# Kernel optimization log

Hardware: AMD Instinct MI355X
Metric: run time of the kernel (lower is better)

Reference implementation:

```python
import jax, jax.numpy as jnp
import numpy as np

N, D = 8192, 1024

def setup_inputs() -> dict:
    key = jax.random.key(0)
    ks = jax.random.split(key, 7)
    s = 1.0 / np.sqrt(D)  # mimic nn.Linear init scale
    return {
        "embeddings": jax.random.normal(ks[0], (N, D), jnp.float32),
        "Wq": jax.random.normal(ks[1], (D, D), jnp.float32) * s,
        "bq": jax.random.normal(ks[2], (D,), jnp.float32) * s,
        "Wk": jax.random.normal(ks[3], (D, D), jnp.float32) * s,
        "bk": jax.random.normal(ks[4], (D,), jnp.float32) * s,
        "Wv": jax.random.normal(ks[5], (D, D), jnp.float32) * s,
        "bv": jax.random.normal(ks[6], (D,), jnp.float32) * s,
    }

def reference(embeddings, Wq, bq, Wk, bk, Wv, bv):
    # nn.Linear: y = x @ W^T + b; weights here are stored as [out, in] equivalent (square), use x @ W.T
    q = embeddings @ Wq.T + bq          # [N, D]
    k = embeddings @ Wk.T + bk          # [N, D]
    v = embeddings @ Wv.T + bv          # [N, D]
    scores = q @ k.T                    # [N, N]  (unscaled, as in source)
    attn = jax.nn.softmax(scores, axis=-1)
    out = attn @ v                      # [N, D]
    return out[:, None, :]              # [N, 1, D] matching torch broadcasted-matmul output
```

## Files before the change

kernel.cpp:

```cpp
#include <hip/hip_runtime.h>
#include <hip/hip_fp16.h>
#include <cstdint>
#include <cstddef>

typedef _Float16 half8 __attribute__((ext_vector_type(8)));
typedef _Float16 half4 __attribute__((ext_vector_type(4)));
typedef float floatx16 __attribute__((ext_vector_type(16)));

#define N_TOK 8192
#define DIM   1024

#define EPI_F32   0
#define EPI_PART  1

__device__ __forceinline__ void async_tile16(const _Float16* gp, _Float16* lp) {
    __builtin_amdgcn_global_load_lds(
        (const __attribute__((address_space(1))) void*)gp,
        (__attribute__((address_space(3))) void*)lp, 16, 0, 0);
}

template<int BM, int BN, int BK, bool ASPLIT, int EPI, bool REMAP>
__global__ __launch_bounds__(256)
void gemm_f16(const _Float16* __restrict__ Ahi, const _Float16* __restrict__ Alo,
              const _Float16* __restrict__ B,
              int kslice, int lda, int ldb,
              float* __restrict__ C, int ldc)
{
    constexpr int MI = BM / 64;
    constexpr int NI = BN / 64;
    constexpr int CPR = BK / 8;
    constexpr int SW  = CPR - 1;
    constexpr int RPP = 2048 / BK;
    constexpr int IA  = BM * BK / 2048;
    constexpr int IB  = BN * BK / 2048;
    constexpr int A_ELTS = BM * BK;
    constexpr int B_ELTS = BN * BK;
    __shared__ _Float16 smem[(ASPLIT ? 2 : 1) * A_ELTS + B_ELTS];
    constexpr int tAhi = 0;
    constexpr int tAlo = A_ELTS;
    constexpr int tB   = (ASPLIT ? 2 : 1) * A_ELTS;

    int bx = blockIdx.x, by = blockIdx.y, bz = blockIdx.z;
    if constexpr (REMAP) {
        const int gx = gridDim.x, gy = gridDim.y;
        const int gxy = gx * gy;
        const int nb = gxy * gridDim.z;
        const int bid = bz * gxy + by * gx + bx;
        const int nid = (bid & 7) * (nb >> 3) + (bid >> 3);
        bx = nid % gx; by = (nid / gx) % gy; bz = nid / gxy;
    }

    const int tid  = threadIdx.x;
    const int row0 = by * BM;
    const int col0 = bx * BN;
    const int lane = tid & 63;
    const int w    = tid >> 6;
    const int wm   = w & 1, wn = w >> 1;
    const int l31  = lane & 31, lhi = lane >> 5;

    floatx16 acc[MI][NI];
#pragma unroll
    for (int mi = 0; mi < MI; mi++)
#pragma unroll
        for (int ni = 0; ni < NI; ni++)
#pragma unroll
            for (int e = 0; e < 16; e++) acc[mi][ni][e] = 0.f;

    const int r_s = tid / CPR;
    const int j_s = tid % CPR;

    const int k_beg = bz * kslice;
    for (int k0 = k_beg; k0 < k_beg + kslice; k0 += BK) {
        __syncthreads();
#pragma unroll
        for (int i = 0; i < IA; i++) {
            const int r = i * RPP + r_s;
            const int jg = j_s ^ ((r >> 1) & SW);
            async_tile16(Ahi + (size_t)(row0 + r) * lda + k0 + jg * 8,
                         smem + tAhi + (i * 256 + tid) * 8);
            if constexpr (ASPLIT)
                async_tile16(Alo + (size_t)(row0 + r) * lda + k0 + jg * 8,
                             smem + tAlo + (i * 256 + tid) * 8);
        }
#pragma unroll
        for (int i = 0; i < IB; i++) {
            const int r = i * RPP + r_s;
            const int jg = j_s ^ ((r >> 1) & SW);
            async_tile16(B + (size_t)(col0 + r) * ldb + k0 + jg * 8,
                         smem + tB + (i * 256 + tid) * 8);
        }
        __syncthreads();

#pragma unroll
        for (int ks = 0; ks < BK / 16; ks++) {
            half8 af[MI], bf[NI];
            half8 al[ASPLIT ? MI : 1];
            const int cb = ks * 2 + lhi;
#pragma unroll
            for (int mi = 0; mi < MI; mi++) {
                const int r = wm * (BM / 2) + mi * 32 + l31;
                const int cj = (cb ^ ((r >> 1) & SW)) * 8;
                af[mi] = *(half8*)&smem[tAhi + r * BK + cj];
                if constexpr (ASPLIT) al[mi] = *(half8*)&smem[tAlo + r * BK + cj];
            }
#pragma unroll
            for (int ni = 0; ni < NI; ni++) {
                const int r = wn * (BN / 2) + ni * 32 + l31;
                const int cj = (cb ^ ((r >> 1) & SW)) * 8;
                bf[ni] = *(half8*)&smem[tB + r * BK + cj];
            }
#pragma unroll
            for (int mi = 0; mi < MI; mi++)
#pragma unroll
                for (int ni = 0; ni < NI; ni++) {
                    acc[mi][ni] = __builtin_amdgcn_mfma_f32_32x32x16_f16(af[mi], bf[ni], acc[mi][ni], 0, 0, 0);
                    if constexpr (ASPLIT)
                        acc[mi][ni] = __builtin_amdgcn_mfma_f32_32x32x16_f16(al[mi], bf[ni], acc[mi][ni], 0, 0, 0);
                }
        }
    }

#pragma unroll
    for (int mi = 0; mi < MI; mi++) {
#pragma unroll
        for (int ni = 0; ni < NI; ni++) {
            const int colg = col0 + wn * (BN / 2) + ni * 32 + l31;
            const int base = row0 + wm * (BM / 2) + mi * 32 + 4 * lhi;
#pragma unroll
            for (int g = 0; g < 4; g++) {
                const int rowb = base + 8 * g;
#pragma unroll
                for (int r2 = 0; r2 < 4; r2++) {
                    const int rowg = rowb + r2;
                    const float v = acc[mi][ni][4 * g + r2];
                    if constexpr (EPI == EPI_F32) {
                        C[(size_t)rowg * ldc + colg] = v;
                    } else {
                        C[(size_t)rowg * ldc + (size_t)bz * DIM + colg] = v;
                    }
                }
            }
        }
    }
}

template<int BM, int BN, int BK>
__global__ __launch_bounds__(256)
void gemm_qkv(const _Float16* __restrict__ Ehi, const _Float16* __restrict__ Elo,
              const _Float16* __restrict__ W,
              _Float16* __restrict__ qhi, _Float16* __restrict__ qlo,
              _Float16* __restrict__ khi, _Float16* __restrict__ vtr,
              const float* __restrict__ bq, const float* __restrict__ bk,
              const float* __restrict__ bv)
{
    constexpr int MI = BM / 64;
    constexpr int NI = BN / 64;
    constexpr int CPR = BK / 8;
    constexpr int SW  = CPR - 1;
    constexpr int RPP = 2048 / BK;
    constexpr int IA  = BM * BK / 2048;
    constexpr int IB  = BN * BK / 2048;
    constexpr int A_ELTS = BM * BK;
    constexpr int B_ELTS = BN * BK;
    __shared__ _Float16 smem[2 * A_ELTS + B_ELTS];
    constexpr int tAhi = 0;
    constexpr int tAlo = A_ELTS;
    constexpr int tB   = 2 * A_ELTS;

    int bx = blockIdx.x, by = blockIdx.y, bz = blockIdx.z;
    {
        const int gx = gridDim.x, gy = gridDim.y;
        const int gxy = gx * gy;
        const int nb = gxy * gridDim.z;
        const int bid = bz * gxy + by * gx + bx;
        const int nid = (bid & 7) * (nb >> 3) + (bid >> 3);
        bx = nid % gx; by = (nid / gx) % gy; bz = nid / gxy;
    }
    const int unit = bz;
    const bool dolo = (unit < 2);

    const int tid  = threadIdx.x;
    const int row0 = by * BM;
    const int col0 = bx * BN;
    const int lane = tid & 63;
    const int w    = tid >> 6;
    const int wm   = w & 1, wn = w >> 1;
    const int l31  = lane & 31, lhi = lane >> 5;

    floatx16 acc[MI][NI];
#pragma unroll
    for (int mi = 0; mi < MI; mi++)
#pragma unroll
        for (int ni = 0; ni < NI; ni++)
#pragma unroll
            for (int e = 0; e < 16; e++) acc[mi][ni][e] = 0.f;

    const int r_s = tid / CPR;
    const int j_s = tid % CPR;
    const size_t brow0 = (size_t)(unit * DIM + col0);

    for (int k0 = 0; k0 < DIM; k0 += BK) {
        __syncthreads();
#pragma unroll
        for (int i = 0; i < IA; i++) {
            const int r = i * RPP + r_s;
            const int jg = j_s ^ ((r >> 1) & SW);
            async_tile16(Ehi + (size_t)(row0 + r) * DIM + k0 + jg * 8,
                         smem + tAhi + (i * 256 + tid) * 8);
            if (dolo)
                async_tile16(Elo + (size_t)(row0 + r) * DIM + k0 + jg * 8,
                             smem + tAlo + (i * 256 + tid) * 8);
        }
#pragma unroll
        for (int i = 0; i < IB; i++) {
            const int r = i * RPP + r_s;
            const int jg = j_s ^ ((r >> 1) & SW);
            async_tile16(W + (brow0 + r) * DIM + k0 + jg * 8,
                         smem + tB + (i * 256 + tid) * 8);
        }
        __syncthreads();

#pragma unroll
        for (int ks = 0; ks < BK / 16; ks++) {
            half8 af[MI], bf[NI], al[MI];
            const int cb = ks * 2 + lhi;
#pragma unroll
            for (int mi = 0; mi < MI; mi++) {
                const int r = wm * (BM / 2) + mi * 32 + l31;
                const int cj = (cb ^ ((r >> 1) & SW)) * 8;
                af[mi] = *(half8*)&smem[tAhi + r * BK + cj];
                if (dolo) al[mi] = *(half8*)&smem[tAlo + r * BK + cj];
            }
#pragma unroll
            for (int ni = 0; ni < NI; ni++) {
                const int r = wn * (BN / 2) + ni * 32 + l31;
                const int cj = (cb ^ ((r >> 1) & SW)) * 8;
                bf[ni] = *(half8*)&smem[tB + r * BK + cj];
            }
#pragma unroll
            for (int mi = 0; mi < MI; mi++)
#pragma unroll
                for (int ni = 0; ni < NI; ni++)
                    acc[mi][ni] = __builtin_amdgcn_mfma_f32_32x32x16_f16(af[mi], bf[ni], acc[mi][ni], 0, 0, 0);
            if (dolo) {
#pragma unroll
                for (int mi = 0; mi < MI; mi++)
#pragma unroll
                    for (int ni = 0; ni < NI; ni++)
                        acc[mi][ni] = __builtin_amdgcn_mfma_f32_32x32x16_f16(al[mi], bf[ni], acc[mi][ni], 0, 0, 0);
            }
        }
    }

    const float* bias = (unit == 0) ? bq : (unit == 1) ? bk : bv;
#pragma unroll
    for (int mi = 0; mi < MI; mi++) {
#pragma unroll
        for (int ni = 0; ni < NI; ni++) {
            const int colg = col0 + wn * (BN / 2) + ni * 32 + l31;
            const float bb = bias[colg];
            const int base = row0 + wm * (BM / 2) + mi * 32 + 4 * lhi;
#pragma unroll
            for (int g = 0; g < 4; g++) {
                const int rowb = base + 8 * g;
                if (unit == 2) {
                    half4 hv;
#pragma unroll
                    for (int r2 = 0; r2 < 4; r2++) hv[r2] = (_Float16)(acc[mi][ni][4 * g + r2] + bb);
                    *(half4*)&vtr[(size_t)colg * N_TOK + rowb] = hv;
                } else {
#pragma unroll
                    for (int r2 = 0; r2 < 4; r2++) {
                        const int rowg = rowb + r2;
                        const float t = acc[mi][ni][4 * g + r2] + bb;
                        const _Float16 hi = (_Float16)t;
                        if (unit == 0) {
                            qhi[(size_t)rowg * DIM + colg] = hi;
                            qlo[(size_t)rowg * DIM + colg] = (_Float16)(t - (float)hi);
                        } else {
                            khi[(size_t)rowg * DIM + colg] = hi;
                        }
                    }
                }
            }
        }
    }
}

__global__ __launch_bounds__(256)
void split_inputs(const float* __restrict__ E,
                  const float* __restrict__ Wq, const float* __restrict__ Wk, const float* __restrict__ Wv,
                  _Float16* __restrict__ Ehi, _Float16* __restrict__ Elo,
                  _Float16* __restrict__ Wqh, _Float16* __restrict__ Wkh, _Float16* __restrict__ Wvh)
{
    const int u = blockIdx.y;
    const size_t idx = ((size_t)blockIdx.x * 256 + threadIdx.x) * 4;
    const size_t MM = (size_t)DIM * DIM;
    const float* src; _Float16* dhi; _Float16* dlo = nullptr;
    if (u < 8)      { src = E + u * MM;  dhi = Ehi + u * MM; dlo = Elo + u * MM; }
    else if (u == 8){ src = Wq; dhi = Wqh; }
    else if (u == 9){ src = Wk; dhi = Wkh; }
    else            { src = Wv; dhi = Wvh; }
    const float4 f = *(const float4*)(src + idx);
    half4 hh;
    hh[0] = (_Float16)f.x; hh[1] = (_Float16)f.y; hh[2] = (_Float16)f.z; hh[3] = (_Float16)f.w;
    *(half4*)(dhi + idx) = hh;
    if (u < 8) {
        half4 hl;
        hl[0] = (_Float16)(f.x - (float)hh[0]); hl[1] = (_Float16)(f.y - (float)hh[1]);
        hl[2] = (_Float16)(f.z - (float)hh[2]); hl[3] = (_Float16)(f.w - (float)hh[3]);
        *(half4*)(dlo + idx) = hl;
    }
}

__global__ __launch_bounds__(256)
void softmax_rows(float* __restrict__ S, float* __restrict__ inv_l)
{
    __shared__ float srow[N_TOK];
    __shared__ float red[4];
    const int tid = threadIdx.x;
    float* row = S + (size_t)blockIdx.x * N_TOK;

    float mx = -3.0e38f;
#pragma unroll
    for (int i = 0; i < 8; i++) {
        const int v = i * 256 + tid;
        const float4 f = ((const float4*)row)[v];
        ((float4*)srow)[v] = f;
        mx = fmaxf(mx, fmaxf(fmaxf(f.x, f.y), fmaxf(f.z, f.w)));
    }
#pragma unroll
    for (int off = 32; off > 0; off >>= 1) mx = fmaxf(mx, __shfl_down(mx, off));
    if ((tid & 63) == 0) red[tid >> 6] = mx;
    __syncthreads();
    mx = fmaxf(fmaxf(red[0], red[1]), fmaxf(red[2], red[3]));
    __syncthreads();

    float sum = 0.f;
    _Float16* prow = (_Float16*)row;
#pragma unroll
    for (int i = 0; i < 8; i++) {
        const int v = i * 256 + tid;
        const float4 f = ((const float4*)srow)[v];
        const float e0 = __expf(f.x - mx), e1 = __expf(f.y - mx);
        const float e2 = __expf(f.z - mx), e3 = __expf(f.w - mx);
        sum += (e0 + e1) + (e2 + e3);
        half4 h; h[0] = (_Float16)e0; h[1] = (_Float16)e1; h[2] = (_Float16)e2; h[3] = (_Float16)e3;
        ((half4*)prow)[v] = h;
    }
#pragma unroll
    for (int off = 32; off > 0; off >>= 1) sum += __shfl_down(sum, off);
    if ((tid & 63) == 0) red[tid >> 6] = sum;
    __syncthreads();
    if (tid == 0) inv_l[blockIdx.x] = 1.f / (red[0] + red[1] + red[2] + red[3]);
}

__global__ __launch_bounds__(256)
void reduce_pv(const float* __restrict__ Sc, const float* __restrict__ invl,
               float* __restrict__ out)
{
    const int r  = blockIdx.x;
    const int c4 = threadIdx.x;
    const float* p = Sc + (size_t)r * N_TOK + N_TOK / 2 + (size_t)c4 * 4;
    float4 s = *(const float4*)p;
#pragma unroll
    for (int z = 1; z < 4; z++) {
        const float4 t = *(const float4*)(p + (size_t)z * DIM);
        s.x += t.x; s.y += t.y; s.z += t.z; s.w += t.w;
    }
    const float iv = invl[r];
    float4 o; o.x = s.x * iv; o.y = s.y * iv; o.z = s.z * iv; o.w = s.w * iv;
    *(float4*)(out + (size_t)r * DIM + (size_t)c4 * 4) = o;
}

extern "C" void kernel_launch(void* const* d_in, const int* in_sizes, int n_in,
                              void* d_out, int out_size, void* d_ws, size_t ws_size,
                              hipStream_t stream)
{
    const float* E  = (const float*)d_in[0];
    const float* Wq = (const float*)d_in[1];
    const float* bq = (const float*)d_in[2];
    const float* Wk = (const float*)d_in[3];
    const float* bk = (const float*)d_in[4];
    const float* Wv = (const float*)d_in[5];
    const float* bv = (const float*)d_in[6];
    float* out = (float*)d_out;

    char* ws = (char*)d_ws;
    const size_t SZ = (size_t)N_TOK * DIM * sizeof(_Float16);
    const size_t WW = (size_t)DIM * DIM * sizeof(_Float16);
    _Float16* q_hi = (_Float16*)(ws);
    _Float16* q_lo = (_Float16*)(ws + SZ);
    _Float16* k_hi = (_Float16*)(ws + 2 * SZ);
    _Float16* vt   = (_Float16*)(ws + 3 * SZ);
    float*    invl = (float*)(ws + 4 * SZ);
    char*     scratch = ws + 4 * SZ + 65536;
    _Float16* Ehi = (_Float16*)(scratch);
    _Float16* Elo = (_Float16*)(scratch + SZ);
    _Float16* Wqh = (_Float16*)(scratch + 2 * SZ);
    _Float16* Wkh = (_Float16*)(scratch + 2 * SZ + WW);
    _Float16* Wvh = (_Float16*)(scratch + 2 * SZ + 2 * WW);
    float*    Sc  = (float*)(scratch);
    const size_t esplit_bytes = 2 * SZ + 3 * WW;
    const size_t base = 4 * SZ + 65536;

    int NC = 256;
    const int cands[6] = {8192, 4096, 2048, 1024, 512, 256};
    for (int i = 0; i < 6; i++) {
        size_t sc = (size_t)cands[i] * N_TOK * 4;
        size_t need = base + (sc > esplit_bytes ? sc : esplit_bytes);
        if (ws_size >= need) { NC = cands[i]; break; }
    }

    const dim3 blk(256, 1, 1);
    constexpr int KS = 4;

    split_inputs<<<dim3(DIM * DIM / 1024, 11, 1), blk, 0, stream>>>(
        E, Wq, Wk, Wv, Ehi, Elo, Wqh, Wkh, Wvh);

    gemm_qkv<128, 128, 64><<<dim3(DIM / 128, N_TOK / 128, 3), blk, 0, stream>>>(
        Ehi, Elo, Wqh, q_hi, q_lo, k_hi, vt, bq, bk, bv);

    const int nchunks = N_TOK / NC;
    for (int c = 0; c < nchunks; c++) {
        const size_t roff = (size_t)c * NC;
        gemm_f16<128, 128, 64, true, EPI_F32, false><<<dim3(N_TOK / 128, NC / 128, 1), blk, 0, stream>>>(
            q_hi + roff * DIM, q_lo + roff * DIM, k_hi, DIM, DIM, DIM, Sc, N_TOK);
        softmax_rows<<<dim3(NC, 1, 1), blk, 0, stream>>>(Sc, invl + roff);
        gemm_f16<128, 128, 64, false, EPI_PART, true><<<dim3(DIM / 128, NC / 128, KS), blk, 0, stream>>>(
            (const _Float16*)Sc, nullptr, vt, N_TOK / KS, 2 * N_TOK, N_TOK,
            Sc + N_TOK / 2, N_TOK);
        reduce_pv<<<dim3(NC, 1, 1), blk, 0, stream>>>(Sc, invl + roff, out + roff * DIM);
    }
}
```

Measured before the change: 721.2 us.

## Replace score and PV GEMMs with 256x256 double-buffered 8-wave MFMA kernel

```diff
diff --git a/kernel.cpp b/kernel.cpp
--- a/kernel.cpp
+++ b/kernel.cpp
@@ -5,6 +5,7 @@
 
 typedef _Float16 half8 __attribute__((ext_vector_type(8)));
 typedef _Float16 half4 __attribute__((ext_vector_type(4)));
+typedef float floatx4 __attribute__((ext_vector_type(4)));
 typedef float floatx16 __attribute__((ext_vector_type(16)));
 
 #define N_TOK 8192
@@ -12,6 +13,10 @@
 
 #define EPI_F32   0
 #define EPI_PART  1
+
+#define FENCE_BARRIER() asm volatile("s_barrier" ::: "memory")
+#define WAIT_VM4()      asm volatile("s_waitcnt vmcnt(4)" ::: "memory")
+#define WAIT_VM0()      asm volatile("s_waitcnt vmcnt(0)" ::: "memory")
 
 __device__ __forceinline__ void async_tile16(const _Float16* gp, _Float16* lp) {
     __builtin_amdgcn_global_load_lds(
@@ -19,26 +24,13 @@
         (__attribute__((address_space(3))) void*)lp, 16, 0, 0);
 }
 
-template<int BM, int BN, int BK, bool ASPLIT, int EPI, bool REMAP>
-__global__ __launch_bounds__(256)
-void gemm_f16(const _Float16* __restrict__ Ahi, const _Float16* __restrict__ Alo,
-              const _Float16* __restrict__ B,
-              int kslice, int lda, int ldb,
-              float* __restrict__ C, int ldc)
-{
-    constexpr int MI = BM / 64;
-    constexpr int NI = BN / 64;
-    constexpr int CPR = BK / 8;
-    constexpr int SW  = CPR - 1;
-    constexpr int RPP = 2048 / BK;
-    constexpr int IA  = BM * BK / 2048;
-    constexpr int IB  = BN * BK / 2048;
-    constexpr int A_ELTS = BM * BK;
-    constexpr int B_ELTS = BN * BK;
-    __shared__ _Float16 smem[(ASPLIT ? 2 : 1) * A_ELTS + B_ELTS];
-    constexpr int tAhi = 0;
-    constexpr int tAlo = A_ELTS;
-    constexpr int tB   = (ASPLIT ? 2 : 1) * A_ELTS;
+template<int EPI, bool FOLD, bool REMAP>
+__global__ __launch_bounds__(512)
+void gemm8(const _Float16* __restrict__ Ahi, const _Float16* __restrict__ Alo,
+           const _Float16* __restrict__ B, int lda, int ldb, int ntiles,
+           float* __restrict__ C, int ldc)
+{
+    __shared__ _Float16 smem[65536];
 
     int bx = blockIdx.x, by = blockIdx.y, bz = blockIdx.z;
     if constexpr (REMAP) {
@@ -51,93 +43,133 @@
     }
 
     const int tid  = threadIdx.x;
-    const int row0 = by * BM;
-    const int col0 = bx * BN;
     const int lane = tid & 63;
     const int w    = tid >> 6;
-    const int wm   = w & 1, wn = w >> 1;
-    const int l31  = lane & 31, lhi = lane >> 5;
-
-    floatx16 acc[MI][NI];
-#pragma unroll
-    for (int mi = 0; mi < MI; mi++)
-#pragma unroll
-        for (int ni = 0; ni < NI; ni++)
-#pragma unroll
-            for (int e = 0; e < 16; e++) acc[mi][ni][e] = 0.f;
-
-    const int r_s = tid / CPR;
-    const int j_s = tid % CPR;
-
-    const int k_beg = bz * kslice;
-    for (int k0 = k_beg; k0 < k_beg + kslice; k0 += BK) {
-        __syncthreads();
-#pragma unroll
-        for (int i = 0; i < IA; i++) {
-            const int r = i * RPP + r_s;
-            const int jg = j_s ^ ((r >> 1) & SW);
-            async_tile16(Ahi + (size_t)(row0 + r) * lda + k0 + jg * 8,
-                         smem + tAhi + (i * 256 + tid) * 8);
-            if constexpr (ASPLIT)
-                async_tile16(Alo + (size_t)(row0 + r) * lda + k0 + jg * 8,
-                             smem + tAlo + (i * 256 + tid) * 8);
-        }
-#pragma unroll
-        for (int i = 0; i < IB; i++) {
-            const int r = i * RPP + r_s;
-            const int jg = j_s ^ ((r >> 1) & SW);
-            async_tile16(B + (size_t)(col0 + r) * ldb + k0 + jg * 8,
-                         smem + tB + (i * 256 + tid) * 8);
-        }
-        __syncthreads();
-
-#pragma unroll
-        for (int ks = 0; ks < BK / 16; ks++) {
-            half8 af[MI], bf[NI];
-            half8 al[ASPLIT ? MI : 1];
-            const int cb = ks * 2 + lhi;
-#pragma unroll
-            for (int mi = 0; mi < MI; mi++) {
-                const int r = wm * (BM / 2) + mi * 32 + l31;
-                const int cj = (cb ^ ((r >> 1) & SW)) * 8;
-                af[mi] = *(half8*)&smem[tAhi + r * BK + cj];
-                if constexpr (ASPLIT) al[mi] = *(half8*)&smem[tAlo + r * BK + cj];
-            }
-#pragma unroll
-            for (int ni = 0; ni < NI; ni++) {
-                const int r = wn * (BN / 2) + ni * 32 + l31;
-                const int cj = (cb ^ ((r >> 1) & SW)) * 8;
-                bf[ni] = *(half8*)&smem[tB + r * BK + cj];
-            }
-#pragma unroll
-            for (int mi = 0; mi < MI; mi++)
-#pragma unroll
-                for (int ni = 0; ni < NI; ni++) {
-                    acc[mi][ni] = __builtin_amdgcn_mfma_f32_32x32x16_f16(af[mi], bf[ni], acc[mi][ni], 0, 0, 0);
-                    if constexpr (ASPLIT)
-                        acc[mi][ni] = __builtin_amdgcn_mfma_f32_32x32x16_f16(al[mi], bf[ni], acc[mi][ni], 0, 0, 0);
-                }
-        }
-    }
-
-#pragma unroll
-    for (int mi = 0; mi < MI; mi++) {
-#pragma unroll
-        for (int ni = 0; ni < NI; ni++) {
-            const int colg = col0 + wn * (BN / 2) + ni * 32 + l31;
-            const int base = row0 + wm * (BM / 2) + mi * 32 + 4 * lhi;
-#pragma unroll
-            for (int g = 0; g < 4; g++) {
-                const int rowb = base + 8 * g;
-#pragma unroll
-                for (int r2 = 0; r2 < 4; r2++) {
-                    const int rowg = rowb + r2;
-                    const float v = acc[mi][ni][4 * g + r2];
-                    if constexpr (EPI == EPI_F32) {
-                        C[(size_t)rowg * ldc + colg] = v;
-                    } else {
-                        C[(size_t)rowg * ldc + (size_t)bz * DIM + colg] = v;
-                    }
+    const int wm   = w >> 2;
+    const int wn   = w & 3;
+    const int l15  = lane & 15;
+    const int l4   = lane >> 4;
+    const int row0 = by * 256;
+    const int col0 = bx * 256;
+    const int kbeg_t = FOLD ? 0 : bz * ntiles;
+
+    const int r_s = tid >> 3;
+    const int j_s = tid & 7;
+
+    _Float16* A0 = smem;
+    _Float16* B0 = smem + 16384;
+    _Float16* A1 = smem + 32768;
+    _Float16* B1 = smem + 49152;
+
+    const int co0 = ((l4)     ^ (l15 >> 1)) << 3;
+    const int co1 = ((4 + l4) ^ (l15 >> 1)) << 3;
+
+    floatx4 acc[8][4];
+#pragma unroll
+    for (int mi = 0; mi < 8; mi++)
+#pragma unroll
+        for (int ni = 0; ni < 4; ni++)
+#pragma unroll
+            for (int e = 0; e < 4; e++) acc[mi][ni][e] = 0.f;
+
+    half8 af[4][2], bf[4][2];
+
+    auto asrc = [&](int kt) -> const _Float16* {
+        int ktc = kt > ntiles - 1 ? ntiles - 1 : kt;
+        if constexpr (FOLD) {
+            const _Float16* base = (ktc < 16) ? Ahi : Alo;
+            return base + (size_t)row0 * lda + (ktc & 15) * 64;
+        } else {
+            return Ahi + (size_t)row0 * lda + (size_t)(kbeg_t + ktc) * 64;
+        }
+    };
+    auto bsrc = [&](int kt) -> const _Float16* {
+        int ktc = kt > ntiles - 1 ? ntiles - 1 : kt;
+        const int kk = FOLD ? (ktc & 15) : (kbeg_t + ktc);
+        return B + (size_t)col0 * ldb + (size_t)kk * 64;
+    };
+
+    auto stage = [&](const _Float16* tile, int ld, int half, _Float16* reg) {
+#pragma unroll
+        for (int p = 0; p < 2; p++) {
+            const int r  = half * 128 + p * 64 + r_s;
+            const int jg = j_s ^ ((r >> 1) & 7);
+            async_tile16(tile + (size_t)r * ld + jg * 8, reg + r * 64 + j_s * 8);
+        }
+    };
+
+    auto lda4 = [&](const _Float16* Ab, int mbase) {
+#pragma unroll
+        for (int m2 = 0; m2 < 4; m2++) {
+            const int r = (wm * 128 + (mbase + m2) * 16 + l15) * 64;
+            af[m2][0] = *(const half8*)&Ab[r + co0];
+            af[m2][1] = *(const half8*)&Ab[r + co1];
+        }
+    };
+    auto ldb2 = [&](const _Float16* Bb, int nbase) {
+#pragma unroll
+        for (int n2 = 0; n2 < 2; n2++) {
+            const int r = (wn * 64 + (nbase + n2) * 16 + l15) * 64;
+            bf[nbase + n2][0] = *(const half8*)&Bb[r + co0];
+            bf[nbase + n2][1] = *(const half8*)&Bb[r + co1];
+        }
+    };
+    auto quad = [&](int qm, int qn) {
+        __builtin_amdgcn_s_setprio(1);
+#pragma unroll
+        for (int m2 = 0; m2 < 4; m2++)
+#pragma unroll
+            for (int n2 = 0; n2 < 2; n2++)
+#pragma unroll
+                for (int kk = 0; kk < 2; kk++)
+                    acc[qm * 4 + m2][qn * 2 + n2] =
+                        __builtin_amdgcn_mfma_f32_16x16x32_f16(
+                            af[m2][kk], bf[qn * 2 + n2][kk],
+                            acc[qm * 4 + m2][qn * 2 + n2], 0, 0, 0);
+        __builtin_amdgcn_s_setprio(0);
+    };
+
+    stage(bsrc(0), ldb, 0, B0); stage(bsrc(0), ldb, 1, B0);
+    stage(asrc(0), lda, 0, A0); stage(asrc(0), lda, 1, A0);
+    stage(bsrc(1), ldb, 0, B1); stage(bsrc(1), ldb, 1, B1);
+    WAIT_VM4();
+    FENCE_BARRIER();
+
+    const int NIc = ntiles >> 1;
+    for (int i = 0; i < NIc; i++) {
+        const int t1 = 2 * i + 1, t2 = 2 * i + 2, t3 = 2 * i + 3;
+        ldb2(B0, 0); lda4(A0, 0); stage(asrc(t1), lda, 0, A1);
+        FENCE_BARRIER(); quad(0, 0); FENCE_BARRIER();
+        ldb2(B0, 2); stage(asrc(t1), lda, 1, A1);
+        FENCE_BARRIER(); quad(0, 1); FENCE_BARRIER();
+        lda4(A0, 4); stage(bsrc(t2), ldb, 0, B0);
+        FENCE_BARRIER(); quad(1, 0); FENCE_BARRIER();
+        stage(bsrc(t2), ldb, 1, B0);
+        FENCE_BARRIER(); quad(1, 1); WAIT_VM4(); FENCE_BARRIER();
+        ldb2(B1, 0); lda4(A1, 0); stage(asrc(t2), lda, 0, A0);
+        FENCE_BARRIER(); quad(0, 0); FENCE_BARRIER();
+        ldb2(B1, 2); stage(asrc(t2), lda, 1, A0);
+        FENCE_BARRIER(); quad(0, 1); FENCE_BARRIER();
+        lda4(A1, 4); stage(bsrc(t3), ldb, 0, B1);
+        FENCE_BARRIER(); quad(1, 0); FENCE_BARRIER();
+        stage(bsrc(t3), ldb, 1, B1);
+        FENCE_BARRIER(); quad(1, 1); WAIT_VM4(); FENCE_BARRIER();
+    }
+    WAIT_VM0();
+
+#pragma unroll
+    for (int mi = 0; mi < 8; mi++) {
+#pragma unroll
+        for (int ni = 0; ni < 4; ni++) {
+            const int row = row0 + wm * 128 + mi * 16 + l4 * 4;
+            const int col = col0 + wn * 64 + ni * 16 + l15;
+#pragma unroll
+            for (int r2 = 0; r2 < 4; r2++) {
+                const float v = acc[mi][ni][r2];
+                if constexpr (EPI == EPI_F32) {
+                    C[(size_t)(row + r2) * ldc + col] = v;
+                } else {
+                    C[(size_t)(row + r2) * ldc + (size_t)bz * DIM + col] = v;
                 }
             }
         }
@@ -413,6 +445,7 @@
     }
 
     const dim3 blk(256, 1, 1);
+    const dim3 blk512(512, 1, 1);
     constexpr int KS = 4;
 
     split_inputs<<<dim3(DIM * DIM / 1024, 11, 1), blk, 0, stream>>>(
@@ -424,12 +457,11 @@
     const int nchunks = N_TOK / NC;
     for (int c = 0; c < nchunks; c++) {
         const size_t roff = (size_t)c * NC;
-        gemm_f16<128, 128, 64, true, EPI_F32, false><<<dim3(N_TOK / 128, NC / 128, 1), blk, 0, stream>>>(
-            q_hi + roff * DIM, q_lo + roff * DIM, k_hi, DIM, DIM, DIM, Sc, N_TOK);
+        gemm8<EPI_F32, true, true><<<dim3(N_TOK / 256, NC / 256, 1), blk512, 0, stream>>>(
+            q_hi + roff * DIM, q_lo + roff * DIM, k_hi, DIM, DIM, 32, Sc, N_TOK);
         softmax_rows<<<dim3(NC, 1, 1), blk, 0, stream>>>(Sc, invl + roff);
-        gemm_f16<128, 128, 64, false, EPI_PART, true><<<dim3(DIM / 128, NC / 128, KS), blk, 0, stream>>>(
-            (const _Float16*)Sc, nullptr, vt, N_TOK / KS, 2 * N_TOK, N_TOK,
-            Sc + N_TOK / 2, N_TOK);
+        gemm8<EPI_PART, false, true><<<dim3(DIM / 256, NC / 256, KS), blk512, 0, stream>>>(
+            (const _Float16*)Sc, nullptr, vt, 2 * N_TOK, N_TOK, 32, Sc + N_TOK / 2, N_TOK);
         reduce_pv<<<dim3(NC, 1, 1), blk, 0, stream>>>(Sc, invl + roff, out + roff * DIM);
     }
 }
```

After: 680.2 us. -5.7%, faster.
